# Kernel optimization log

Measured on AMD Instinct MI355X. Metric: run time of the kernel, lower is better.

The kernel has to match this reference:

```python
import jax, jax.numpy as jnp
import numpy as np

B, H, N, P = 2, 8, 2048, 64   # batch, heads, seq, head_dim
M, D = 4, 256                 # sketch count, sketch feature dim


def setup_inputs() -> dict:
    key = jax.random.key(0)
    kq, kk, ks, kr = jax.random.split(key, 4)
    scale = P ** -0.5  # keep exp(QK) numerically tame, std(dot) ~= 1/8
    Q = jax.random.normal(kq, (B, H, N, P), dtype=jnp.float32) * scale
    K = jax.random.normal(kk, (B, H, N, P), dtype=jnp.float32) * scale
    # indices into the concatenated [Q;K] token axis of length 2N
    sketching_matrix = jax.random.randint(ks, (B, M, D), 0, 2 * N)
    # Rademacher random signs, broadcast over [b,h,2n] in the reduction
    random_sign = jnp.sign(jax.random.normal(kr, (M, D), dtype=jnp.float32))
    random_sign = jnp.where(random_sign == 0, 1.0, random_sign)
    return {"Q": Q, "K": K, "sketching_matrix": sketching_matrix,
            "random_sign": random_sign}


def reference(Q, K, sketching_matrix, random_sign):
    b, h, n, p = Q.shape
    X = jnp.concatenate([Q, K], axis=2)          # [b,h,2n,p]
    Xt = jnp.transpose(X, (0, 2, 1, 3))          # [b,2n,h,p]
    # gather sketched landmarks: [b,m,d,h,p] -> [b,h,m,d,p]
    XS = Xt[jnp.arange(b)[:, None, None], sketching_matrix]
    XS = jnp.transpose(XS, (0, 3, 1, 2, 4))
    # RS_SM accumulate branch: exp of inner products, random-sign reduce over m
    product = jnp.einsum('bhnp,bhmdp->bhnmd', X, XS)   # [b,h,2n,m,d]
    AS = jnp.einsum('bhnmd,md->bhnd', jnp.exp(product), random_sign)
    return AS.astype(Q.dtype)                    # [b,h,2n,d]
```

## Files before the change

kernel.cpp:

```cpp
#include <hip/hip_runtime.h>
#include <hip/hip_bf16.h>

typedef __attribute__((ext_vector_type(8))) short short8;
typedef __attribute__((ext_vector_type(4))) float f32x4;

namespace {
constexpr int Nc  = 2048;
constexpr int NXc = 4096;
constexpr int Pc  = 64;
constexpr int Mc  = 4;
constexpr int Dc  = 256;
constexpr int BH  = 16;
constexpr float LOG2E = 1.4426950408889634f;
}

__device__ inline float fexp2(float x) {
#if __has_builtin(__builtin_amdgcn_exp2f)
  return __builtin_amdgcn_exp2f(x);
#else
  return exp2f(x);
#endif
}

__device__ inline unsigned int bfpack(float a, float b) {
  union { __hip_bfloat162 h; unsigned int u; } cv;
  cv.h = __float22bfloat162_rn(make_float2(a, b));
  return cv.u;
}

__global__ __launch_bounds__(256) void prepass_kernel(
    const float* __restrict__ Q, const float* __restrict__ K,
    const int* __restrict__ SK, __hip_bfloat16* __restrict__ Wb)
{
  const int t  = blockIdx.x * 256 + threadIdx.x;
  const int q  = t & 7;
  const int r  = t >> 3;
  const int bh = r >> 10;
  const int md = r & 1023;
  const int b  = bh >> 3;
  const int idx = SK[b * (Mc * Dc) + md];
  const float* src = (idx < Nc) ? (Q + ((size_t)bh * Nc + idx) * Pc)
                                : (K + ((size_t)bh * Nc + (idx - Nc)) * Pc);
  const f32x4* s4 = (const f32x4*)(src + q * 8);
  f32x4 f0 = s4[0], f1 = s4[1];
  uint4 u;
  u.x = bfpack(f0.x * LOG2E, f0.y * LOG2E);
  u.y = bfpack(f0.z * LOG2E, f0.w * LOG2E);
  u.z = bfpack(f1.x * LOG2E, f1.y * LOG2E);
  u.w = bfpack(f1.z * LOG2E, f1.w * LOG2E);
  *(uint4*)(Wb + (size_t)r * Pc + q * 8) = u;
}

__global__ __launch_bounds__(256, 4) void sketch_main(
    const float* __restrict__ Q, const float* __restrict__ K,
    const __hip_bfloat16* __restrict__ Wb,
    const float* __restrict__ SGN, float* __restrict__ OUT)
{
  __shared__ __hip_bfloat16 Ws[Mc * 64 * Pc];

  const int t    = threadIdx.x;
  const int lane = t & 63;
  const int wv   = t >> 6;
  const int brow = lane & 15;
  const int q    = lane >> 4;
  const int bh   = blockIdx.y;

  const int bx  = blockIdx.x;
  const int xcd = bx & 7;
  const int rr  = bx >> 3;
  const int nch = xcd * 2 + (rr >> 2);
  const int dq  = rr & 3;
  const int n0  = nch * 256;
  const int d0  = dq * 64;

  char* wsb = (char*)Ws;

  {
    const int dl = t >> 2;
    const int qt = t & 3;
    const int sw = (dl & 7) << 4;
    const __hip_bfloat16* wsrc =
        Wb + ((size_t)bh * (Mc * Dc) + d0 + dl) * Pc + qt * 16;
    #pragma unroll
    for (int m = 0; m < 4; ++m) {
      uint4 wa = *(const uint4*)(wsrc + (size_t)m * Dc * Pc);
      uint4 wb = *(const uint4*)(wsrc + (size_t)m * Dc * Pc + 8);
      char* rp = wsb + (m * 64 + dl) * 128;
      *(uint4*)(rp + ((qt * 32) ^ sw))      = wa;
      *(uint4*)(rp + ((qt * 32 + 16) ^ sw)) = wb;
    }
  }

  const float* xr = ((n0 < Nc) ? (Q + ((size_t)bh * Nc + n0) * Pc)
                               : (K + ((size_t)bh * Nc + (n0 - Nc)) * Pc))
                    + (size_t)(wv * 64 + brow) * Pc + q * 8;
  f32x4 xv[16];
  #pragma unroll
  for (int tt = 0; tt < 4; ++tt) {
    const float* xp = xr + (size_t)tt * 16 * Pc;
    xv[tt * 4 + 0] = *(const f32x4*)(xp);
    xv[tt * 4 + 1] = *(const f32x4*)(xp + 4);
    xv[tt * 4 + 2] = *(const f32x4*)(xp + 32);
    xv[tt * 4 + 3] = *(const f32x4*)(xp + 36);
  }

  __syncthreads();

  short8 b0[4], b1[4];
  #pragma unroll
  for (int tt = 0; tt < 4; ++tt) {
    union { short8 s; uint4 u; } c0, c1;
    f32x4 x0 = xv[tt * 4 + 0], x1 = xv[tt * 4 + 1];
    f32x4 x2 = xv[tt * 4 + 2], x3 = xv[tt * 4 + 3];
    c0.u.x = bfpack(x0.x, x0.y); c0.u.y = bfpack(x0.z, x0.w);
    c0.u.z = bfpack(x1.x, x1.y); c0.u.w = bfpack(x1.z, x1.w);
    c1.u.x = bfpack(x2.x, x2.y); c1.u.y = bfpack(x2.z, x2.w);
    c1.u.z = bfpack(x3.x, x3.y); c1.u.w = bfpack(x3.z, x3.w);
    b0[tt] = c0.s; b1[tt] = c1.s;
  }

  const int swr = (brow & 7) << 4;
  float* obase = OUT + ((size_t)bh * NXc + n0 + wv * 64 + brow) * Dc + d0 + q * 4;

  #pragma unroll
  for (int dt = 0; dt < 4; ++dt) {
    f32x4 acc[4];
    #pragma unroll
    for (int tt = 0; tt < 4; ++tt) acc[tt] = (f32x4){0.f, 0.f, 0.f, 0.f};

    #pragma unroll
    for (int m = 0; m < 4; ++m) {
      const char* ap = wsb + (m * 64 + dt * 16 + brow) * 128;
      short8 a0 = *(const short8*)(ap + ((q * 16) ^ swr));
      short8 a1 = *(const short8*)(ap + ((64 + q * 16) ^ swr));
      const f32x4 sg = *(const f32x4*)(SGN + m * Dc + d0 + dt * 16 + q * 4);
      #pragma unroll
      for (int tt = 0; tt < 4; ++tt) {
        f32x4 c = {0.f, 0.f, 0.f, 0.f};
        c = __builtin_amdgcn_mfma_f32_16x16x32_bf16(a0, b0[tt], c, 0, 0, 0);
        c = __builtin_amdgcn_mfma_f32_16x16x32_bf16(a1, b1[tt], c, 0, 0, 0);
        acc[tt].x = fmaf(sg.x, fexp2(c.x), acc[tt].x);
        acc[tt].y = fmaf(sg.y, fexp2(c.y), acc[tt].y);
        acc[tt].z = fmaf(sg.z, fexp2(c.z), acc[tt].z);
        acc[tt].w = fmaf(sg.w, fexp2(c.w), acc[tt].w);
      }
    }

    #pragma unroll
    for (int tt = 0; tt < 4; ++tt) {
      __builtin_nontemporal_store(
          acc[tt], (f32x4*)(obase + (size_t)tt * 16 * Dc + dt * 16));
    }
  }
}

extern "C" void kernel_launch(void* const* d_in, const int* in_sizes, int n_in,
                              void* d_out, int out_size, void* d_ws, size_t ws_size,
                              hipStream_t stream) {
  (void)in_sizes; (void)n_in; (void)out_size; (void)ws_size;
  const float* Q   = (const float*)d_in[0];
  const float* K   = (const float*)d_in[1];
  const int*   SK  = (const int*)d_in[2];
  const float* SGN = (const float*)d_in[3];
  float* OUT = (float*)d_out;

  __hip_bfloat16* Wb = (__hip_bfloat16*)d_ws;

  prepass_kernel<<<dim3(512), dim3(256), 0, stream>>>(Q, K, SK, Wb);
  sketch_main<<<dim3(64, BH), dim3(256), 0, stream>>>(Q, K, Wb, SGN, OUT);
}
```

Baseline: 106.5 us.

## Halve per-block d tile and split row tiles to raise occupancy

```diff
diff --git a/kernel.cpp b/kernel.cpp
--- a/kernel.cpp
+++ b/kernel.cpp
@@ -51,12 +51,12 @@
   *(uint4*)(Wb + (size_t)r * Pc + q * 8) = u;
 }
 
-__global__ __launch_bounds__(256, 4) void sketch_main(
+__global__ __launch_bounds__(256, 6) void sketch_main(
     const float* __restrict__ Q, const float* __restrict__ K,
     const __hip_bfloat16* __restrict__ Wb,
     const float* __restrict__ SGN, float* __restrict__ OUT)
 {
-  __shared__ __hip_bfloat16 Ws[Mc * 64 * Pc];
+  __shared__ __hip_bfloat16 Ws[Mc * 32 * Pc];
 
   const int t    = threadIdx.x;
   const int lane = t & 63;
@@ -68,36 +68,39 @@
   const int bx  = blockIdx.x;
   const int xcd = bx & 7;
   const int rr  = bx >> 3;
-  const int nch = xcd * 2 + (rr >> 2);
-  const int dq  = rr & 3;
+  const int nch = xcd * 2 + (rr >> 3);
+  const int dq  = rr & 7;
   const int n0  = nch * 256;
-  const int d0  = dq * 64;
+  const int d0  = dq * 32;
 
   char* wsb = (char*)Ws;
 
   {
-    const int dl = t >> 2;
     const int qt = t & 3;
-    const int sw = (dl & 7) << 4;
-    const __hip_bfloat16* wsrc =
-        Wb + ((size_t)bh * (Mc * Dc) + d0 + dl) * Pc + qt * 16;
+    const int r4 = t >> 2;
     #pragma unroll
-    for (int m = 0; m < 4; ++m) {
-      uint4 wa = *(const uint4*)(wsrc + (size_t)m * Dc * Pc);
-      uint4 wb = *(const uint4*)(wsrc + (size_t)m * Dc * Pc + 8);
-      char* rp = wsb + (m * 64 + dl) * 128;
+    for (int p = 0; p < 2; ++p) {
+      const int row = p * 64 + r4;
+      const int m  = row >> 5;
+      const int dl = row & 31;
+      const __hip_bfloat16* wsrc =
+          Wb + ((size_t)bh * (Mc * Dc) + m * Dc + d0 + dl) * Pc + qt * 16;
+      uint4 wa = *(const uint4*)(wsrc);
+      uint4 wb = *(const uint4*)(wsrc + 8);
+      char* rp = wsb + row * 128;
+      const int sw = (row & 7) << 4;
       *(uint4*)(rp + ((qt * 32) ^ sw))      = wa;
       *(uint4*)(rp + ((qt * 32 + 16) ^ sw)) = wb;
     }
   }
 
-  const float* xr = ((n0 < Nc) ? (Q + ((size_t)bh * Nc + n0) * Pc)
-                               : (K + ((size_t)bh * Nc + (n0 - Nc)) * Pc))
-                    + (size_t)(wv * 64 + brow) * Pc + q * 8;
-  f32x4 xv[16];
+  const float* xrw = ((n0 < Nc) ? (Q + ((size_t)bh * Nc + n0) * Pc)
+                                : (K + ((size_t)bh * Nc + (n0 - Nc)) * Pc))
+                     + (size_t)(wv * 64 + brow) * Pc + q * 8;
+  f32x4 xv[8];
   #pragma unroll
-  for (int tt = 0; tt < 4; ++tt) {
-    const float* xp = xr + (size_t)tt * 16 * Pc;
+  for (int tt = 0; tt < 2; ++tt) {
+    const float* xp = xrw + (size_t)tt * 16 * Pc;
     xv[tt * 4 + 0] = *(const f32x4*)(xp);
     xv[tt * 4 + 1] = *(const f32x4*)(xp + 4);
     xv[tt * 4 + 2] = *(const f32x4*)(xp + 32);
@@ -106,50 +109,69 @@
 
   __syncthreads();
 
-  short8 b0[4], b1[4];
-  #pragma unroll
-  for (int tt = 0; tt < 4; ++tt) {
-    union { short8 s; uint4 u; } c0, c1;
-    f32x4 x0 = xv[tt * 4 + 0], x1 = xv[tt * 4 + 1];
-    f32x4 x2 = xv[tt * 4 + 2], x3 = xv[tt * 4 + 3];
-    c0.u.x = bfpack(x0.x, x0.y); c0.u.y = bfpack(x0.z, x0.w);
-    c0.u.z = bfpack(x1.x, x1.y); c0.u.w = bfpack(x1.z, x1.w);
-    c1.u.x = bfpack(x2.x, x2.y); c1.u.y = bfpack(x2.z, x2.w);
-    c1.u.z = bfpack(x3.x, x3.y); c1.u.w = bfpack(x3.z, x3.w);
-    b0[tt] = c0.s; b1[tt] = c1.s;
-  }
-
   const int swr = (brow & 7) << 4;
   float* obase = OUT + ((size_t)bh * NXc + n0 + wv * 64 + brow) * Dc + d0 + q * 4;
 
   #pragma unroll
-  for (int dt = 0; dt < 4; ++dt) {
-    f32x4 acc[4];
+  for (int pr = 0; pr < 2; ++pr) {
+    if (pr == 1) {
+      #pragma unroll
+      for (int tt = 0; tt < 2; ++tt) {
+        const float* xp = xrw + (size_t)(2 + tt) * 16 * Pc;
+        xv[tt * 4 + 0] = *(const f32x4*)(xp);
+        xv[tt * 4 + 1] = *(const f32x4*)(xp + 4);
+        xv[tt * 4 + 2] = *(const f32x4*)(xp + 32);
+        xv[tt * 4 + 3] = *(const f32x4*)(xp + 36);
+      }
+    }
+    short8 b0[2], b1[2];
     #pragma unroll
-    for (int tt = 0; tt < 4; ++tt) acc[tt] = (f32x4){0.f, 0.f, 0.f, 0.f};
+    for (int tt = 0; tt < 2; ++tt) {
+      union { short8 s; uint4 u; } c0, c1;
+      f32x4 x0 = xv[tt * 4 + 0], x1 = xv[tt * 4 + 1];
+      f32x4 x2 = xv[tt * 4 + 2], x3 = xv[tt * 4 + 3];
+      c0.u.x = bfpack(x0.x, x0.y); c0.u.y = bfpack(x0.z, x0.w);
+      c0.u.z = bfpack(x1.x, x1.y); c0.u.w = bfpack(x1.z, x1.w);
+      c1.u.x = bfpack(x2.x, x2.y); c1.u.y = bfpack(x2.z, x2.w);
+      c1.u.z = bfpack(x3.x, x3.y); c1.u.w = bfpack(x3.z, x3.w);
+      b0[tt] = c0.s; b1[tt] = c1.s;
+    }
+
+    f32x4 acc[2][2];
+    #pragma unroll
+    for (int tt = 0; tt < 2; ++tt)
+      #pragma unroll
+      for (int dt = 0; dt < 2; ++dt) acc[tt][dt] = (f32x4){0.f, 0.f, 0.f, 0.f};
 
     #pragma unroll
-    for (int m = 0; m < 4; ++m) {
-      const char* ap = wsb + (m * 64 + dt * 16 + brow) * 128;
-      short8 a0 = *(const short8*)(ap + ((q * 16) ^ swr));
-      short8 a1 = *(const short8*)(ap + ((64 + q * 16) ^ swr));
-      const f32x4 sg = *(const f32x4*)(SGN + m * Dc + d0 + dt * 16 + q * 4);
+    for (int dt = 0; dt < 2; ++dt) {
       #pragma unroll
-      for (int tt = 0; tt < 4; ++tt) {
-        f32x4 c = {0.f, 0.f, 0.f, 0.f};
-        c = __builtin_amdgcn_mfma_f32_16x16x32_bf16(a0, b0[tt], c, 0, 0, 0);
-        c = __builtin_amdgcn_mfma_f32_16x16x32_bf16(a1, b1[tt], c, 0, 0, 0);
-        acc[tt].x = fmaf(sg.x, fexp2(c.x), acc[tt].x);
-        acc[tt].y = fmaf(sg.y, fexp2(c.y), acc[tt].y);
-        acc[tt].z = fmaf(sg.z, fexp2(c.z), acc[tt].z);
-        acc[tt].w = fmaf(sg.w, fexp2(c.w), acc[tt].w);
+      for (int m = 0; m < 4; ++m) {
+        const char* ap = wsb + (m * 32 + dt * 16 + brow) * 128;
+        short8 a0 = *(const short8*)(ap + ((q * 16) ^ swr));
+        short8 a1 = *(const short8*)(ap + ((64 + q * 16) ^ swr));
+        const f32x4 sg = *(const f32x4*)(SGN + m * Dc + d0 + dt * 16 + q * 4);
+        #pragma unroll
+        for (int tt = 0; tt < 2; ++tt) {
+          f32x4 c = {0.f, 0.f, 0.f, 0.f};
+          c = __builtin_amdgcn_mfma_f32_16x16x32_bf16(a0, b0[tt], c, 0, 0, 0);
+          c = __builtin_amdgcn_mfma_f32_16x16x32_bf16(a1, b1[tt], c, 0, 0, 0);
+          acc[tt][dt].x = fmaf(sg.x, fexp2(c.x), acc[tt][dt].x);
+          acc[tt][dt].y = fmaf(sg.y, fexp2(c.y), acc[tt][dt].y);
+          acc[tt][dt].z = fmaf(sg.z, fexp2(c.z), acc[tt][dt].z);
+          acc[tt][dt].w = fmaf(sg.w, fexp2(c.w), acc[tt][dt].w);
+        }
       }
     }
 
     #pragma unroll
-    for (int tt = 0; tt < 4; ++tt) {
-      __builtin_nontemporal_store(
-          acc[tt], (f32x4*)(obase + (size_t)tt * 16 * Dc + dt * 16));
+    for (int tt = 0; tt < 2; ++tt) {
+      #pragma unroll
+      for (int dt = 0; dt < 2; ++dt) {
+        __builtin_nontemporal_store(
+            acc[tt][dt],
+            (f32x4*)(obase + (size_t)(pr * 2 + tt) * 16 * Dc + dt * 16));
+      }
     }
   }
 }
@@ -167,5 +189,5 @@
   __hip_bfloat16* Wb = (__hip_bfloat16*)d_ws;
 
   prepass_kernel<<<dim3(512), dim3(256), 0, stream>>>(Q, K, SK, Wb);
-  sketch_main<<<dim3(64, BH), dim3(256), 0, stream>>>(Q, K, Wb, SGN, OUT);
+  sketch_main<<<dim3(128, BH), dim3(256), 0, stream>>>(Q, K, Wb, SGN, OUT);
 }
```

After: 116.9 us. 9.8% more time.
